# Kernel tuning notes

Measured on AMD Instinct MI355X. Metric: run time of the kernel, lower is better.

## Reference

```python
import jax, jax.numpy as jnp
import numpy as np

N_NODES = 100000


def gcn_layer(x, ei, W, b):
    # PyG GCNConv with add_self_loops=True, edge_weight=None (all ones)
    N = x.shape[0]
    loops = jnp.arange(N, dtype=ei.dtype)
    src = jnp.concatenate([ei[0], loops])
    dst = jnp.concatenate([ei[1], loops])
    h = x @ W  # [N, out_dim]
    ones = jnp.ones(src.shape[0], dtype=x.dtype)
    deg = jax.ops.segment_sum(ones, dst, num_segments=N)
    dinv = jnp.where(deg > 0, jax.lax.rsqrt(deg), 0.0)
    norm = dinv[src] * dinv[dst]  # [E+N]
    msgs = norm[:, None] * h[src]
    out = jax.ops.segment_sum(msgs, dst, num_segments=N)
    return out + b


def forward_once(x, ei, W1, b1, W2, b2):
    h = jax.nn.relu(gcn_layer(x, ei, W1, b1))
    # Dropout(0.25) is identity in eval mode
    z = gcn_layer(h, ei, W2, b2)
    return z  # [N, embed_dim]


def setup_inputs() -> dict:
    key = jax.random.key(0)
    k = jax.random.split(key, 6)
    feat_dim, hidden_dim, embed_dim = 128, 32, 16
    R, E = 4, 1600000
    x = jax.random.normal(k[0], (N_NODES, feat_dim), dtype=jnp.float32)
    eis = jax.random.randint(k[1], (R, 2, E), 0, N_NODES, dtype=jnp.int32)
    s1 = 1.0 / np.sqrt(feat_dim)
    s2 = 1.0 / np.sqrt(hidden_dim)
    W1 = jax.random.uniform(k[2], (feat_dim, hidden_dim), jnp.float32, -s1, s1)
    b1 = jax.random.uniform(k[3], (hidden_dim,), jnp.float32, -s1, s1)
    W2 = jax.random.uniform(k[4], (hidden_dim, embed_dim), jnp.float32, -s2, s2)
    b2 = jax.random.uniform(k[5], (embed_dim,), jnp.float32, -s2, s2)
    return {"x": x, "eis": eis, "W1": W1, "b1": b1, "W2": W2, "b2": b2}


def reference(x, eis, W1, b1, W2, b2):
    # vectorize the per-relation loop over the leading R axis of eis
    embeds = jax.vmap(lambda ei: forward_once(x, ei, W1, b1, W2, b2))(eis)
    # default reduce: embeds.sum(dim=2) on [R, N, embed_dim] -> [R, N]
    return embeds.sum(axis=2)
```

## Files before the change

kernel.cpp:

```cpp
#include <hip/hip_runtime.h>


constexpr int N    = 100000;
constexpr int E    = 1600000;
constexpr int R    = 4;
constexpr int FEAT = 128;
constexpr int HID  = 32;
constexpr int EMB  = 16;
constexpr int M    = R * N;
constexpr int BS   = 256;
constexpr int SH    = 9;
constexpr int BSPAN = 1 << SH;
constexpr int NBUCK = (N + BSPAN - 1) / BSPAN;
constexpr int CH    = 4096;
constexpr int EPT   = CH / BS;
constexpr int NBKr  = (E + CH - 1) / CH;
constexpr int RB    = R * NBUCK;
constexpr int CAP   = 8960;
constexpr int FIX   = 16;
constexpr int GNB   = 64;
constexpr int XPITCH = 132;

typedef _Float16 half8 __attribute__((ext_vector_type(8)));
typedef _Float16 half2v __attribute__((ext_vector_type(2)));

__global__ __launch_bounds__(BS)
void k_gemm_h0(const float* __restrict__ x, const float* __restrict__ W1,
               _Float16* __restrict__ H0h) {
    __shared__ float xs[GNB * XPITCH];
    int base = blockIdx.x * GNB;
    int tid  = threadIdx.x;
#pragma unroll
    for (int u = 0; u < 8; ++u) {
        int f = tid + u * BS;
        int n = f >> 5;
        int c = f & 31;
        if (base + n < N) {
            float4 v = ((const float4*)(x + (size_t)(base + n) * FEAT))[c];
            int p = c ^ ((n & 7) << 2);
            *(float4*)&xs[n * XPITCH + p * 4] = v;
        }
    }
    __syncthreads();
    int oct = __builtin_amdgcn_readfirstlane(tid >> 6);
    int l   = tid & 63;
    int i   = base + l;
    const float* wp = W1 + oct * 8;
    float acc[8];
#pragma unroll
    for (int kk = 0; kk < 8; ++kk) acc[kk] = 0.f;
#pragma unroll 4
    for (int c = 0; c < 32; ++c) {
        int p = c ^ ((l & 7) << 2);
        float4 xv = *(const float4*)&xs[l * XPITCH + p * 4];
        float xk[4] = {xv.x, xv.y, xv.z, xv.w};
#pragma unroll
        for (int dk = 0; dk < 4; ++dk) {
            const float* wr = wp + (c * 4 + dk) * HID;
#pragma unroll
            for (int j = 0; j < 8; ++j)
                acc[j] = fmaf(xk[dk], wr[j], acc[j]);
        }
    }
    half8 hv;
#pragma unroll
    for (int kk = 0; kk < 8; ++kk) hv[kk] = (_Float16)acc[kk];
    if (i < N) ((half8*)H0h)[i * 4 + oct] = hv;
}

__global__ void k_wrow(const float* __restrict__ W2, const float* __restrict__ b2,
                       float* __restrict__ wrowbuf) {
    int j = threadIdx.x;
    if (j < HID) {
        float s = 0.f;
#pragma unroll
        for (int k = 0; k < EMB; ++k) s += W2[j * EMB + k];
        wrowbuf[j] = s;
    } else if (j == HID) {
        float s = 0.f;
#pragma unroll
        for (int k = 0; k < EMB; ++k) s += b2[k];
        wrowbuf[HID] = s;
    }
}

__global__ void k_scat2(const int* __restrict__ eis, int* __restrict__ gcur,
                        int* __restrict__ binned) {
    __shared__ int hist[NBUCK], lstart[NBUCK], cursor[NBUCK], gbase[NBUCK];
    __shared__ int wpart[BS / 64];
    __shared__ int shuf[CH];
    __shared__ unsigned char bkt[CH];
    int r = blockIdx.x / NBKr, k = blockIdx.x - r * NBKr;
    const int* srcp = eis + (size_t)r * 2 * E;
    const int* dstp = srcp + E;
    int e0 = k * CH, n = min(CH, E - e0);
    int tid = threadIdx.x;

    int dreg[EPT], sreg[EPT];
    if (n == CH) {
#pragma unroll
        for (int u = 0; u < EPT; ++u) {
            dreg[u] = dstp[e0 + tid + u * BS];
            sreg[u] = srcp[e0 + tid + u * BS];
        }
    } else {
#pragma unroll
        for (int u = 0; u < EPT; ++u) {
            int i = tid + u * BS;
            dreg[u] = (i < n) ? dstp[e0 + i] : -1;
            sreg[u] = (i < n) ? srcp[e0 + i] : 0;
        }
    }
    for (int b = tid; b < NBUCK; b += BS) hist[b] = 0;
    __syncthreads();
#pragma unroll
    for (int u = 0; u < EPT; ++u)
        if (dreg[u] >= 0) atomicAdd(&hist[dreg[u] >> SH], 1);
    __syncthreads();
    int v = (tid < NBUCK) ? hist[tid] : 0;
    int lanei = tid & 63;
    int s = v;
#pragma unroll
    for (int d = 1; d < 64; d <<= 1) {
        int xup = __shfl_up(s, d, 64);
        s += (lanei >= d) ? xup : 0;
    }
    if (lanei == 63) wpart[tid >> 6] = s;
    __syncthreads();
    int offw = 0;
#pragma unroll
    for (int ww = 0; ww < BS / 64; ++ww)
        offw += (ww < (tid >> 6)) ? wpart[ww] : 0;
    int ex = offw + s - v;
    if (tid < NBUCK) {
        lstart[tid] = ex;
        cursor[tid] = ex;
        gbase[tid] = atomicAdd(&gcur[r * NBUCK + tid], v);
    }
    __syncthreads();
#pragma unroll
    for (int u = 0; u < EPT; ++u) {
        int d = dreg[u];
        if (d >= 0) {
            int b = d >> SH;
            int pos = atomicAdd(&cursor[b], 1);
            shuf[pos] = ((d & (BSPAN - 1)) << 17) | sreg[u];
            bkt[pos]  = (unsigned char)b;
        }
    }
    __syncthreads();
    for (int i = tid; i < n; i += BS) {
        int b = bkt[i];
        int pos = gbase[b] + (i - lstart[b]);
        if (pos < CAP)
            binned[(size_t)(r * NBUCK + b) * CAP + pos] = shuf[i];
    }
}

__global__ __launch_bounds__(BSPAN)
void k_sort3(const int* __restrict__ gcur, int* __restrict__ binned,
             int* __restrict__ off, int* __restrict__ cnt,
             float* __restrict__ dinv) {
    __shared__ int shuf[CAP];
    __shared__ int hist[BSPAN], cur[BSPAN];
    __shared__ int wpart[BSPAN / 64];
    int gb = blockIdx.x;
    int r = gb / NBUCK, b = gb - r * NBUCK;
    int n = min(gcur[gb], CAP);
    int base = gb * CAP;
    int tid = threadIdx.x;
    hist[tid] = 0;
    for (int i = tid; i < n; i += BSPAN) shuf[i] = binned[base + i];
    __syncthreads();
    for (int i = tid; i < n; i += BSPAN)
        atomicAdd(&hist[((unsigned)shuf[i]) >> 17], 1);
    __syncthreads();
    int v = hist[tid];
    int lanei = tid & 63;
    int s = v;
#pragma unroll
    for (int d = 1; d < 64; d <<= 1) {
        int xup = __shfl_up(s, d, 64);
        s += (lanei >= d) ? xup : 0;
    }
    if (lanei == 63) wpart[tid >> 6] = s;
    __syncthreads();
    int offw = 0;
#pragma unroll
    for (int ww = 0; ww < BSPAN / 64; ++ww)
        offw += (ww < (tid >> 6)) ? wpart[ww] : 0;
    int ex = offw + s - v;
    cur[tid] = ex;
    int node = (b << SH) + tid;
    if (node < N) {
        int ri = r * N + node;
        off[ri] = base + ex;
        cnt[ri] = v;
        dinv[ri] = rsqrtf((float)v + 1.0f);
    }
    __syncthreads();
    for (int i = tid; i < n; i += BSPAN) {
        int rc = shuf[i];
        int pos = atomicAdd(&cur[((unsigned)rc) >> 17], 1);
        binned[base + pos] = rc & 0x1FFFF;
    }
}

__global__ void k_scale(const float* __restrict__ dinv, const half8* __restrict__ H0h,
                        half8* __restrict__ Hsc, const int* __restrict__ off,
                        const int* __restrict__ cnt, const int* __restrict__ binned,
                        int* __restrict__ fixedsrc) {
    int t = blockIdx.x * blockDim.x + threadIdx.x;
    if (t >= (M + 1) * 4) return;
    int ri = t >> 2, c = t & 3;
    half8 o;
    if (ri == M) {
#pragma unroll
        for (int kk = 0; kk < 8; ++kk) o[kk] = (_Float16)0.f;
    } else {
        int i = ri % N;
        float di = dinv[ri];
        half8 h = H0h[i * 4 + c];
#pragma unroll
        for (int kk = 0; kk < 8; ++kk) o[kk] = (_Float16)(di * (float)h[kk]);
        int base = off[ri];
        int nn = min(cnt[ri], FIX);
        const int* bp = binned + base + c * 4;
        int4 w;
        w.x = (c * 4 + 0 < nn) ? bp[0] : 0;
        w.y = (c * 4 + 1 < nn) ? bp[1] : 0;
        w.z = (c * 4 + 2 < nn) ? bp[2] : 0;
        w.w = (c * 4 + 3 < nn) ? bp[3] : 0;
        ((int4*)(fixedsrc + (size_t)ri * FIX))[c] = w;
    }
    Hsc[t] = o;
}

__global__ void k_l1(const int* __restrict__ off, const int* __restrict__ cnt,
                     const int* __restrict__ ssrc, const int* __restrict__ fixedsrc,
                     const float* __restrict__ dinv, const half8* __restrict__ Hsc,
                     const float* __restrict__ b1, const float* __restrict__ wrowbuf,
                     float* __restrict__ q) {
    int t = blockIdx.x * blockDim.x + threadIdx.x;
    int ri = t >> 4;
    if (ri >= M) return;
    int lane = t & 15;
    int c   = lane & 3;
    int sub = lane >> 2;
    int i = ri % N;
    int rbase = ri - i;
    float di = dinv[ri];
    int n = cnt[ri];
    int fs = fixedsrc[(size_t)ri * FIX + lane];
    int base = off[ri];
    half2v acc[4];
    half2v zz = {(_Float16)0.f, (_Float16)0.f};
#pragma unroll
    for (int kk = 0; kk < 4; ++kk) acc[kk] = zz;

    auto procwin = [&](int sbv, int m) {
        for (int bq = 0; bq < 4 && bq * 4 < m; ++bq) {
            int slot = bq * 4 + sub;
            int sj = __shfl(sbv, slot, 16);
            int idx = (slot < m) ? (rbase + sj) : M;
            half8 h = Hsc[(size_t)idx * 4 + c];
#pragma unroll
            for (int kk = 0; kk < 4; ++kk) {
                half2v hp = {h[2 * kk], h[2 * kk + 1]};
                acc[kk] = acc[kk] + hp;
            }
        }
    };

    int sb = (16 + lane < n) ? ssrc[base + 16 + lane] : 0;
    procwin(fs, n);
    for (int k0 = 16; k0 < n; k0 += 16) {
        int sbn = (k0 + 16 + lane < n) ? ssrc[base + k0 + 16 + lane] : 0;
        procwin(sb, n - k0);
        sb = sbn;
    }
#pragma unroll
    for (int o = 4; o <= 8; o <<= 1) {
#pragma unroll
        for (int kk = 0; kk < 4; ++kk) {
            int av = __builtin_bit_cast(int, acc[kk]);
            av = __shfl_xor(av, o, 16);
            acc[kk] = acc[kk] + __builtin_bit_cast(half2v, av);
        }
    }
    half8 hs = Hsc[(size_t)ri * 4 + c];
#pragma unroll
    for (int kk = 0; kk < 4; ++kk) {
        half2v hp = {hs[2 * kk], hs[2 * kk + 1]};
        acc[kk] = acc[kk] + hp;
    }
    float p = 0.f;
#pragma unroll
    for (int kk = 0; kk < 8; ++kk) {
        float av = (float)acc[kk >> 1][kk & 1];
        int j = c * 8 + kk;
        float h1 = fmaf(di, av, b1[j]);
        h1 = fmaxf(h1, 0.f);
        p = fmaf(h1, wrowbuf[j], p);
    }
    p += __shfl_xor(p, 1, 16);
    p += __shfl_xor(p, 2, 16);
    if (lane == 0) q[ri] = di * p;
}

__global__ void k_l2(const int* __restrict__ off, const int* __restrict__ cnt,
                     const int* __restrict__ ssrc, const int* __restrict__ fixedsrc,
                     const float* __restrict__ dinv, const float* __restrict__ q,
                     const float* __restrict__ wrowbuf, float* __restrict__ out) {
    int t = blockIdx.x * blockDim.x + threadIdx.x;
    int ri = t >> 3;
    if (ri >= M) return;
    int lane = t & 7;
    int i = ri % N;
    int rbase = ri - i;
    int n = cnt[ri];
    int f0 = fixedsrc[(size_t)ri * FIX + lane];
    int f1 = fixedsrc[(size_t)ri * FIX + 8 + lane];
    int base = off[ri];
    float val = 0.f;
    if (lane < n)     val += q[rbase + f0];
    if (8 + lane < n) val += q[rbase + f1];
    for (int idx = 16 + lane; idx < n; idx += 8) {
        int s = ssrc[base + idx];
        val += q[rbase + s];
    }
#pragma unroll
    for (int o = 4; o > 0; o >>= 1) val += __shfl_xor(val, o, 8);
    if (lane == 0)
        out[ri] = dinv[ri] * (val + q[ri]) + wrowbuf[HID];
}

extern "C" void kernel_launch(void* const* d_in, const int* in_sizes, int n_in,
                              void* d_out, int out_size, void* d_ws, size_t ws_size,
                              hipStream_t stream) {
    const float* x  = (const float*)d_in[0];
    const int*  eis = (const int*)d_in[1];
    const float* W1 = (const float*)d_in[2];
    const float* b1 = (const float*)d_in[3];
    const float* W2 = (const float*)d_in[4];
    const float* b2 = (const float*)d_in[5];
    float* out = (float*)d_out;

    _Float16* H0h = (_Float16*)d_ws;
    float* dinv   = (float*)d_ws + (size_t)N * HID / 2;
    float* q      = dinv + M;
    int*   off    = (int*)(q + M);
    int*   cnt    = off + M;
    float* wrowbuf = (float*)(cnt + M);
    int*   gcur   = (int*)(wrowbuf + 64);
    int*   binned = gcur + RB;
    _Float16* Hsc = (_Float16*)(binned + (size_t)RB * CAP);
    int* fixedsrc = (int*)(Hsc + (size_t)(M + 1) * HID);

    k_gemm_h0<<<(N + GNB - 1) / GNB, BS, 0, stream>>>(x, W1, H0h);
    k_wrow  <<<1, 64, 0, stream>>>(W2, b2, wrowbuf);
    hipMemsetAsync(gcur, 0, (size_t)RB * sizeof(int), stream);
    k_scat2 <<<R * NBKr, BS, 0, stream>>>(eis, gcur, binned);
    k_sort3 <<<RB, BSPAN, 0, stream>>>(gcur, binned, off, cnt, dinv);
    k_scale <<<((M + 1) * 4 + BS - 1) / BS, BS, 0, stream>>>(dinv, (const half8*)H0h,
                                                             (half8*)Hsc, off, cnt,
                                                             binned, fixedsrc);
    k_l1    <<<(M * 16 + BS - 1) / BS, BS, 0, stream>>>(off, cnt, binned, fixedsrc,
                                                        dinv, (const half8*)Hsc, b1,
                                                        wrowbuf, q);
    k_l2    <<<(M * 8 + BS - 1) / BS, BS, 0, stream>>>(off, cnt, binned, fixedsrc,
                                                       dinv, q, wrowbuf, out);
}
```

Baseline: 335.2 us.

## Fuse scaling and fixed-source extraction into bucket sort kernel

Removes the separate k_scale kernel and does its work inside k_sort3. Sort3 now keeps each bucket's edges in registers instead of LDS, and records the first FIX sources per node in an LDS table during the scatter. It then writes fixedsrc and the dinv-scaled half-precision H rows per node, and the zero sentinel row is written by k_wrow. This saves one launch and avoids re-reading dinv, off, cnt and binned from global memory. In exchange it adds register pressure (SPT=18 values per thread) and a 32KB LDS table, which may reduce occupancy.

```diff
diff --git a/kernel.cpp b/kernel.cpp
--- a/kernel.cpp
+++ b/kernel.cpp
@@ -17,6 +17,7 @@
 constexpr int NBKr  = (E + CH - 1) / CH;
 constexpr int RB    = R * NBUCK;
 constexpr int CAP   = 8960;
+constexpr int SPT   = (CAP + BSPAN - 1) / BSPAN;
 constexpr int FIX   = 16;
 constexpr int GNB   = 64;
 constexpr int XPITCH = 132;
@@ -69,7 +70,7 @@
 }
 
 __global__ void k_wrow(const float* __restrict__ W2, const float* __restrict__ b2,
-                       float* __restrict__ wrowbuf) {
+                       float* __restrict__ wrowbuf, _Float16* __restrict__ Hsc) {
     int j = threadIdx.x;
     if (j < HID) {
         float s = 0.f;
@@ -81,6 +82,8 @@
 #pragma unroll
         for (int k = 0; k < EMB; ++k) s += b2[k];
         wrowbuf[HID] = s;
+    } else if (j >= 34 && j < 50) {
+        ((unsigned*)(Hsc + (size_t)M * HID))[j - 34] = 0u;
     }
 }
 
@@ -160,20 +163,27 @@
 __global__ __launch_bounds__(BSPAN)
 void k_sort3(const int* __restrict__ gcur, int* __restrict__ binned,
              int* __restrict__ off, int* __restrict__ cnt,
-             float* __restrict__ dinv) {
-    __shared__ int shuf[CAP];
-    __shared__ int hist[BSPAN], cur[BSPAN];
+             float* __restrict__ dinv, const half8* __restrict__ H0h,
+             half8* __restrict__ Hsc, int* __restrict__ fixedsrc) {
+    __shared__ int fix_lds[FIX * BSPAN];
+    __shared__ int hist[BSPAN], cur[BSPAN], exs[BSPAN];
     __shared__ int wpart[BSPAN / 64];
     int gb = blockIdx.x;
     int r = gb / NBUCK, b = gb - r * NBUCK;
     int n = min(gcur[gb], CAP);
     int base = gb * CAP;
     int tid = threadIdx.x;
+    int rg[SPT];
+#pragma unroll
+    for (int u = 0; u < SPT; ++u) {
+        int i = tid + u * BSPAN;
+        rg[u] = (i < n) ? binned[base + i] : -1;
+    }
     hist[tid] = 0;
-    for (int i = tid; i < n; i += BSPAN) shuf[i] = binned[base + i];
-    __syncthreads();
-    for (int i = tid; i < n; i += BSPAN)
-        atomicAdd(&hist[((unsigned)shuf[i]) >> 17], 1);
+    __syncthreads();
+#pragma unroll
+    for (int u = 0; u < SPT; ++u)
+        if (rg[u] >= 0) atomicAdd(&hist[((unsigned)rg[u]) >> 17], 1);
     __syncthreads();
     int v = hist[tid];
     int lanei = tid & 63;
@@ -191,49 +201,49 @@
         offw += (ww < (tid >> 6)) ? wpart[ww] : 0;
     int ex = offw + s - v;
     cur[tid] = ex;
+    exs[tid] = ex;
     int node = (b << SH) + tid;
+    int ri = r * N + node;
     if (node < N) {
-        int ri = r * N + node;
         off[ri] = base + ex;
         cnt[ri] = v;
         dinv[ri] = rsqrtf((float)v + 1.0f);
     }
     __syncthreads();
-    for (int i = tid; i < n; i += BSPAN) {
-        int rc = shuf[i];
-        int pos = atomicAdd(&cur[((unsigned)rc) >> 17], 1);
-        binned[base + pos] = rc & 0x1FFFF;
-    }
-}
-
-__global__ void k_scale(const float* __restrict__ dinv, const half8* __restrict__ H0h,
-                        half8* __restrict__ Hsc, const int* __restrict__ off,
-                        const int* __restrict__ cnt, const int* __restrict__ binned,
-                        int* __restrict__ fixedsrc) {
-    int t = blockIdx.x * blockDim.x + threadIdx.x;
-    if (t >= (M + 1) * 4) return;
-    int ri = t >> 2, c = t & 3;
-    half8 o;
-    if (ri == M) {
-#pragma unroll
-        for (int kk = 0; kk < 8; ++kk) o[kk] = (_Float16)0.f;
-    } else {
-        int i = ri % N;
-        float di = dinv[ri];
-        half8 h = H0h[i * 4 + c];
-#pragma unroll
-        for (int kk = 0; kk < 8; ++kk) o[kk] = (_Float16)(di * (float)h[kk]);
-        int base = off[ri];
-        int nn = min(cnt[ri], FIX);
-        const int* bp = binned + base + c * 4;
-        int4 w;
-        w.x = (c * 4 + 0 < nn) ? bp[0] : 0;
-        w.y = (c * 4 + 1 < nn) ? bp[1] : 0;
-        w.z = (c * 4 + 2 < nn) ? bp[2] : 0;
-        w.w = (c * 4 + 3 < nn) ? bp[3] : 0;
-        ((int4*)(fixedsrc + (size_t)ri * FIX))[c] = w;
-    }
-    Hsc[t] = o;
+#pragma unroll
+    for (int u = 0; u < SPT; ++u) {
+        int rc = rg[u];
+        if (rc >= 0) {
+            int nd = ((unsigned)rc) >> 17;
+            int pos = atomicAdd(&cur[nd], 1);
+            int val = rc & 0x1FFFF;
+            binned[base + pos] = val;
+            int k = pos - exs[nd];
+            if (k < FIX) fix_lds[k * BSPAN + nd] = val;
+        }
+    }
+    __syncthreads();
+    if (node < N) {
+        int nn = min(v, FIX);
+#pragma unroll
+        for (int cc = 0; cc < 4; ++cc) {
+            int4 w;
+            w.x = (cc * 4 + 0 < nn) ? fix_lds[(cc * 4 + 0) * BSPAN + tid] : 0;
+            w.y = (cc * 4 + 1 < nn) ? fix_lds[(cc * 4 + 1) * BSPAN + tid] : 0;
+            w.z = (cc * 4 + 2 < nn) ? fix_lds[(cc * 4 + 2) * BSPAN + tid] : 0;
+            w.w = (cc * 4 + 3 < nn) ? fix_lds[(cc * 4 + 3) * BSPAN + tid] : 0;
+            ((int4*)(fixedsrc + (size_t)ri * FIX))[cc] = w;
+        }
+        float di = rsqrtf((float)v + 1.0f);
+#pragma unroll
+        for (int cc = 0; cc < 4; ++cc) {
+            half8 h = H0h[(size_t)node * 4 + cc];
+            half8 o;
+#pragma unroll
+            for (int kk = 0; kk < 8; ++kk) o[kk] = (_Float16)(di * (float)h[kk]);
+            Hsc[(size_t)ri * 4 + cc] = o;
+        }
+    }
 }
 
 __global__ void k_l1(const int* __restrict__ off, const int* __restrict__ cnt,
@@ -358,13 +368,11 @@
     int* fixedsrc = (int*)(Hsc + (size_t)(M + 1) * HID);
 
     k_gemm_h0<<<(N + GNB - 1) / GNB, BS, 0, stream>>>(x, W1, H0h);
-    k_wrow  <<<1, 64, 0, stream>>>(W2, b2, wrowbuf);
+    k_wrow  <<<1, 64, 0, stream>>>(W2, b2, wrowbuf, Hsc);
     hipMemsetAsync(gcur, 0, (size_t)RB * sizeof(int), stream);
     k_scat2 <<<R * NBKr, BS, 0, stream>>>(eis, gcur, binned);
-    k_sort3 <<<RB, BSPAN, 0, stream>>>(gcur, binned, off, cnt, dinv);
-    k_scale <<<((M + 1) * 4 + BS - 1) / BS, BS, 0, stream>>>(dinv, (const half8*)H0h,
-                                                             (half8*)Hsc, off, cnt,
-                                                             binned, fixedsrc);
+    k_sort3 <<<RB, BSPAN, 0, stream>>>(gcur, binned, off, cnt, dinv,
+                                       (const half8*)H0h, (half8*)Hsc, fixedsrc);
     k_l1    <<<(M * 16 + BS - 1) / BS, BS, 0, stream>>>(off, cnt, binned, fixedsrc,
                                                         dinv, (const half8*)Hsc, b1,
                                                         wrowbuf, q);
```

After: 335.1 us. No clear change (-0.0%).
